# Optimization experiments

Measured on AMD Instinct MI355X. Metric: run time of the kernel, lower is better.

Reference implementation:

```python
import jax, jax.numpy as jnp
import numpy as np

B, S, D = 4, 2048, 1024
E, K, H = 8, 2, 4096


def setup_inputs() -> dict:
    key = jax.random.key(0)
    ks = jax.random.split(key, 8)
    sd = 1.0 / np.sqrt(D)
    sh = 1.0 / np.sqrt(H)
    x = jax.random.normal(ks[0], (B, S, D), dtype=jnp.float32)
    gate_w = jax.random.normal(ks[1], (D, E), dtype=jnp.float32) * sd
    gate_b = jnp.zeros((E,), dtype=jnp.float32)
    w1 = jax.random.normal(ks[2], (E, D, H), dtype=jnp.float32) * sd
    b1 = jnp.zeros((E, H), dtype=jnp.float32)
    w2 = jax.random.normal(ks[3], (E, H, D), dtype=jnp.float32) * sh
    b2 = jnp.zeros((E, D), dtype=jnp.float32)
    return {"x": x, "gate_w": gate_w, "gate_b": gate_b,
            "w1": w1, "b1": b1, "w2": w2, "b2": b2}


def reference(x, gate_w, gate_b, w1, b1, w2, b2):
    # gate logits [B,S,E]
    logits = jnp.einsum('bsd,de->bse', x, gate_w) + gate_b
    # top-k over experts, softmax over the k selected (dim=2), in float32
    weights, selected = jax.lax.top_k(logits, K)            # [B,S,K]
    weights = jax.nn.softmax(weights.astype(jnp.float32), axis=-1).astype(x.dtype)
    out = jnp.zeros_like(x)
    for i in range(E):
        # per-token combine weight for expert i (0 if not routed here)
        w_i = jnp.sum(jnp.where(selected == i, weights, 0.0), axis=-1)  # [B,S]
        h = jax.nn.gelu(jnp.einsum('bsd,dh->bsh', x, w1[i]) + b1[i])    # [B,S,H]
        y = jnp.einsum('bsh,hd->bsd', h, w2[i]) + b2[i]                  # [B,S,D]
        out = out + w_i[..., None] * y
    return out
```

## Files before the change

### kernel.cpp

```cpp
#include <hip/hip_runtime.h>
#include <hip/hip_bf16.h>
#include <stdint.h>

#define T_TOK 8192
#define D_DIM 1024
#define E_NUM 8
#define H_DIM 4096
#define WL_MAX 136

typedef short bf16x8 __attribute__((ext_vector_type(8)));
typedef float f32x4 __attribute__((ext_vector_type(4)));
typedef unsigned short usv8 __attribute__((ext_vector_type(8)));

#define AS1 __attribute__((address_space(1)))
#define AS3 __attribute__((address_space(3)))

__device__ __forceinline__ unsigned short f2b(float f) {
  union { float f; uint32_t u; } v; v.f = f;
  uint32_t r = (v.u + 0x7fffu + ((v.u >> 16) & 1u)) >> 16;
  return (unsigned short)r;
}

__device__ __forceinline__ float gelu_tanh(float x) {
  float u = 0.7978845608028654f * (x + 0.044715f * x * x * x);
  u = fminf(fmaxf(u, -15.f), 15.f);
  float e = __expf(2.f * u);
  float t = (e - 1.f) / (e + 1.f);
  return 0.5f * x * (1.f + t);
}

__device__ __forceinline__ void gload_lds16(const void* g, void* l) {
  __builtin_amdgcn_global_load_lds((const AS1 uint32_t*)g, (AS3 uint32_t*)l, 16, 0, 0);
}

__global__ __launch_bounds__(256) void moe_gate_conv(const float* __restrict__ x,
                                                     const float* __restrict__ gw,
                                                     const float* __restrict__ gb,
                                                     unsigned short* __restrict__ xb,
                                                     int2* __restrict__ sel,
                                                     float2* __restrict__ wts,
                                                     int* __restrict__ meta) {
  int lane = threadIdx.x & 63;
  int t = blockIdx.x * 4 + (threadIdx.x >> 6);
  const float* xr = x + (size_t)t * D_DIM;
  unsigned short* xo = xb + (size_t)t * D_DIM;
  float acc[8];
#pragma unroll
  for (int e = 0; e < 8; e++) acc[e] = 0.f;
#pragma unroll
  for (int i = 0; i < 4; i++) {
    int d0 = lane * 4 + i * 256;
    float4 xv = *(const float4*)(xr + d0);
    ushort4 o;
    o.x = f2b(xv.x); o.y = f2b(xv.y); o.z = f2b(xv.z); o.w = f2b(xv.w);
    *(ushort4*)(xo + d0) = o;
    const float* gp = gw + (size_t)d0 * 8;
    float xs[4] = {xv.x, xv.y, xv.z, xv.w};
#pragma unroll
    for (int j = 0; j < 4; j++) {
#pragma unroll
      for (int e = 0; e < 8; e++) acc[e] += xs[j] * gp[j * 8 + e];
    }
  }
#pragma unroll
  for (int off = 32; off > 0; off >>= 1) {
#pragma unroll
    for (int e = 0; e < 8; e++) acc[e] += __shfl_xor(acc[e], off);
  }
  if (lane == 0) {
    float lg[8];
#pragma unroll
    for (int e = 0; e < 8; e++) lg[e] = acc[e] + gb[e];
    int e0 = 0; float b0 = lg[0];
#pragma unroll
    for (int e = 1; e < 8; e++) if (lg[e] > b0) { b0 = lg[e]; e0 = e; }
    int e1 = -1; float b1v = -1e30f;
#pragma unroll
    for (int e = 0; e < 8; e++) if (e != e0 && lg[e] > b1v) { b1v = lg[e]; e1 = e; }
    float d = __expf(b1v - b0);
    float w0 = 1.f / (1.f + d), w1 = d / (1.f + d);
    sel[t] = make_int2(e0, e1);
    wts[t] = make_float2(w0, w1);
    atomicAdd(&meta[e0], 1);
    atomicAdd(&meta[e1], 1);
  }
}

__global__ __launch_bounds__(256) void moe_transpose(const float* __restrict__ in,
                                                     unsigned short* __restrict__ out,
                                                     int R, int C) {
  int e = blockIdx.z;
  int c0 = blockIdx.x * 64, r0 = blockIdx.y * 64;
  __shared__ float tile[64][65];
  const float* ine = in + (size_t)e * R * C;
  unsigned short* oute = out + (size_t)e * R * C;
  int tr = threadIdx.x >> 2;
  int tc4 = (threadIdx.x & 3) * 16;
#pragma unroll
  for (int p = 0; p < 4; p++) {
    int c = tc4 + p * 4;
    float4 v = *(const float4*)(ine + (size_t)(r0 + tr) * C + c0 + c);
    tile[tr][c] = v.x; tile[tr][c + 1] = v.y; tile[tr][c + 2] = v.z; tile[tr][c + 3] = v.w;
  }
  __syncthreads();
#pragma unroll
  for (int p = 0; p < 4; p++) {
    int rr = tc4 + p * 4;
    ushort4 o;
    o.x = f2b(tile[rr + 0][tr]);
    o.y = f2b(tile[rr + 1][tr]);
    o.z = f2b(tile[rr + 2][tr]);
    o.w = f2b(tile[rr + 3][tr]);
    *(ushort4*)(oute + (size_t)(c0 + tr) * R + r0 + rr) = o;
  }
}

__global__ void moe_scan(int* meta, int2* wl) {
  if (threadIdx.x == 0 && blockIdx.x == 0) {
    int o = 0;
    for (int e = 0; e < 8; e++) { meta[8 + e] = o; meta[20 + e] = o; o += meta[e]; }
    meta[16] = o;
    int w = 0;
    for (int e = 0; e < 8; e++)
      for (int m0 = 0; m0 < meta[e]; m0 += 128) wl[w++] = make_int2(e, m0);
    meta[17] = w;
  }
}

__global__ __launch_bounds__(256) void moe_scatter(const int2* __restrict__ sel,
                                                   int* __restrict__ meta,
                                                   int* __restrict__ token_id,
                                                   int2* __restrict__ pos) {
  int t = blockIdx.x * 256 + threadIdx.x;
  if (t >= T_TOK) return;
  int2 s = sel[t];
  int p0 = atomicAdd(&meta[20 + s.x], 1); token_id[p0] = t;
  int p1 = atomicAdd(&meta[20 + s.y], 1); token_id[p1] = t;
  pos[t] = make_int2(p0, p1);
}

__global__ __launch_bounds__(256) void moe_gemm1(const unsigned short* __restrict__ xb,
                                                 const unsigned short* __restrict__ w1t,
                                                 const float* __restrict__ b1,
                                                 const int* __restrict__ meta,
                                                 const int2* __restrict__ wl,
                                                 const int* __restrict__ token_id,
                                                 unsigned short* __restrict__ hbuf) {
  int wi = blockIdx.y;
  if (wi >= meta[17]) return;
  int e = wl[wi].x, m0 = wl[wi].y;
  int seg = meta[8 + e], ne = meta[9 + e] - seg;
  int n0 = blockIdx.x * 128;
  const unsigned short* wB = w1t + (size_t)e * H_DIM * D_DIM;

  __shared__ unsigned short As[2][4096];
  __shared__ unsigned short Bs[2][4096];

  int tid = threadIdx.x, lane = tid & 63, wv = tid >> 6;
  const unsigned short* aptr[2];
  const unsigned short* bptr[2];
#pragma unroll
  for (int q = 0; q < 2; q++) {
    int chunk = (wv + 4 * q) * 64 + lane;
    int row = chunk >> 2;
    int ko = (chunk & 3) * 8;
    int gi = m0 + row; if (gi >= ne) gi = m0;
    int tok = token_id[seg + gi];
    aptr[q] = xb + (size_t)tok * D_DIM + ko;
    bptr[q] = wB + (size_t)(n0 + row) * D_DIM + ko;
  }
  auto stage = [&](int buf, int kt) {
#pragma unroll
    for (int q = 0; q < 2; q++) {
      gload_lds16(aptr[q] + kt * 32, &As[buf][(wv + 4 * q) * 512]);
      gload_lds16(bptr[q] + kt * 32, &Bs[buf][(wv + 4 * q) * 512]);
    }
  };

  f32x4 acc[4][4] = {};
  int wr = wv >> 1, wc = wv & 1;
  int abase = (wr * 64 + (lane & 15)) * 32 + (lane >> 4) * 8;
  int bbase = (wc * 64 + (lane & 15)) * 32 + (lane >> 4) * 8;

  stage(0, 0);
  __syncthreads();
  const int nk = D_DIM / 32;
  for (int kt = 0; kt < nk; ++kt) {
    int cur = kt & 1;
    if (kt + 1 < nk) stage(cur ^ 1, kt + 1);
    bf16x8 af[4], bfr[4];
#pragma unroll
    for (int m = 0; m < 4; m++) af[m] = *(const bf16x8*)&As[cur][abase + m * 512];
#pragma unroll
    for (int n = 0; n < 4; n++) bfr[n] = *(const bf16x8*)&Bs[cur][bbase + n * 512];
#pragma unroll
    for (int m = 0; m < 4; m++)
#pragma unroll
      for (int n = 0; n < 4; n++)
        acc[m][n] = __builtin_amdgcn_mfma_f32_16x16x32_bf16(af[m], bfr[n], acc[m][n], 0, 0, 0);
    __syncthreads();
  }

  int rbase = wr * 64 + (lane >> 4) * 4;
  int cbase = n0 + wc * 64 + (lane & 15);
  const float* b1e = b1 + (size_t)e * H_DIM + cbase;
  float bv[4];
#pragma unroll
  for (int n = 0; n < 4; n++) bv[n] = b1e[n * 16];
#pragma unroll
  for (int m = 0; m < 4; m++) {
#pragma unroll
    for (int j = 0; j < 4; j++) {
      int gi = m0 + rbase + m * 16 + j;
      if (gi < ne) {
        unsigned short* hrow = hbuf + (size_t)(seg + gi) * H_DIM + cbase;
#pragma unroll
        for (int n = 0; n < 4; n++) {
          float v = acc[m][n][j] + bv[n];
          hrow[n * 16] = f2b(gelu_tanh(v));
        }
      }
    }
  }
}

__global__ __launch_bounds__(256) void moe_gemm2(const unsigned short* __restrict__ hbuf,
                                                 const unsigned short* __restrict__ w2t,
                                                 const float* __restrict__ b2,
                                                 const int* __restrict__ meta,
                                                 const int2* __restrict__ wl,
                                                 float* __restrict__ y) {
  int wi = blockIdx.y;
  if (wi >= meta[17]) return;
  int e = wl[wi].x, m0 = wl[wi].y;
  int seg = meta[8 + e], ne = meta[9 + e] - seg;
  int n0 = blockIdx.x * 128;
  const unsigned short* wB = w2t + (size_t)e * D_DIM * H_DIM;

  __shared__ unsigned short As[2][4096];
  __shared__ unsigned short Bs[2][4096];

  int tid = threadIdx.x, lane = tid & 63, wv = tid >> 6;
  const unsigned short* aptr[2];
  const unsigned short* bptr[2];
#pragma unroll
  for (int q = 0; q < 2; q++) {
    int chunk = (wv + 4 * q) * 64 + lane;
    int row = chunk >> 2;
    int ko = (chunk & 3) * 8;
    int gi = m0 + row; if (gi >= ne) gi = m0;
    aptr[q] = hbuf + (size_t)(seg + gi) * H_DIM + ko;
    bptr[q] = wB + (size_t)(n0 + row) * H_DIM + ko;
  }
  auto stage = [&](int buf, int kt) {
#pragma unroll
    for (int q = 0; q < 2; q++) {
      gload_lds16(aptr[q] + kt * 32, &As[buf][(wv + 4 * q) * 512]);
      gload_lds16(bptr[q] + kt * 32, &Bs[buf][(wv + 4 * q) * 512]);
    }
  };

  f32x4 acc[4][4] = {};
  int wr = wv >> 1, wc = wv & 1;
  int abase = (wr * 64 + (lane & 15)) * 32 + (lane >> 4) * 8;
  int bbase = (wc * 64 + (lane & 15)) * 32 + (lane >> 4) * 8;

  stage(0, 0);
  __syncthreads();
  const int nk = H_DIM / 32;
  for (int kt = 0; kt < nk; ++kt) {
    int cur = kt & 1;
    if (kt + 1 < nk) stage(cur ^ 1, kt + 1);
    bf16x8 af[4], bfr[4];
#pragma unroll
    for (int m = 0; m < 4; m++) af[m] = *(const bf16x8*)&As[cur][abase + m * 512];
#pragma unroll
    for (int n = 0; n < 4; n++) bfr[n] = *(const bf16x8*)&Bs[cur][bbase + n * 512];
#pragma unroll
    for (int m = 0; m < 4; m++)
#pragma unroll
      for (int n = 0; n < 4; n++)
        acc[m][n] = __builtin_amdgcn_mfma_f32_16x16x32_bf16(af[m], bfr[n], acc[m][n], 0, 0, 0);
    __syncthreads();
  }

  int rbase = wr * 64 + (lane >> 4) * 4;
  int cbase = n0 + wc * 64 + (lane & 15);
  const float* b2e = b2 + (size_t)e * D_DIM + cbase;
  float bv[4];
#pragma unroll
  for (int n = 0; n < 4; n++) bv[n] = b2e[n * 16];
#pragma unroll
  for (int m = 0; m < 4; m++) {
#pragma unroll
    for (int j = 0; j < 4; j++) {
      int gi = m0 + rbase + m * 16 + j;
      if (gi < ne) {
        float* yrow = y + (size_t)(seg + gi) * D_DIM + cbase;
#pragma unroll
        for (int n = 0; n < 4; n++)
          yrow[n * 16] = acc[m][n][j] + bv[n];
      }
    }
  }
}

__global__ __launch_bounds__(256) void moe_combine(const float* __restrict__ y,
                                                   const int2* __restrict__ pos,
                                                   const float2* __restrict__ wts,
                                                   float* __restrict__ out) {
  int i = blockIdx.x * 256 + threadIdx.x;
  int idx = i * 4;
  int t = idx >> 10, d = idx & 1023;
  int2 p = pos[t];
  float2 w = wts[t];
  float4 a = *(const float4*)(y + (size_t)p.x * D_DIM + d);
  float4 b = *(const float4*)(y + (size_t)p.y * D_DIM + d);
  float4 o;
  o.x = w.x * a.x + w.y * b.x;
  o.y = w.x * a.y + w.y * b.y;
  o.z = w.x * a.z + w.y * b.z;
  o.w = w.x * a.w + w.y * b.w;
  *(float4*)(out + idx) = o;
}

extern "C" void kernel_launch(void* const* d_in, const int* in_sizes, int n_in,
                              void* d_out, int out_size, void* d_ws, size_t ws_size,
                              hipStream_t stream) {
  const float* x      = (const float*)d_in[0];
  const float* gate_w = (const float*)d_in[1];
  const float* gate_b = (const float*)d_in[2];
  const float* w1     = (const float*)d_in[3];
  const float* b1     = (const float*)d_in[4];
  const float* w2     = (const float*)d_in[5];
  const float* b2     = (const float*)d_in[6];
  float* out = (float*)d_out;

  uint8_t* ws = (uint8_t*)d_ws;
  unsigned short* hbuf = (unsigned short*)(ws);
  unsigned short* xb   = (unsigned short*)(ws + 134217728ull);
  unsigned short* w1t  = (unsigned short*)(ws + 150994944ull);
  float*          yb   = (float*)         (ws + 150994944ull);
  unsigned short* w2t  = (unsigned short*)(ws + 218103808ull);
  int*    token_id = (int*)  (ws + 285212672ull);
  int2*   pos      = (int2*) (ws + 285278208ull);
  float2* wts      = (float2*)(ws + 285343744ull);
  int2*   sel      = (int2*) (ws + 285409280ull);
  int*    meta     = (int*)  (ws + 285474816ull);
  int2*   wl       = (int2*) (ws + 285475328ull);

  hipMemsetAsync(meta, 0, 512, stream);

  moe_gate_conv<<<dim3(T_TOK / 4), 256, 0, stream>>>(x, gate_w, gate_b, xb, sel, wts, meta);
  moe_transpose<<<dim3(H_DIM / 64, D_DIM / 64, E_NUM), 256, 0, stream>>>(w1, w1t, D_DIM, H_DIM);
  moe_transpose<<<dim3(D_DIM / 64, H_DIM / 64, E_NUM), 256, 0, stream>>>(w2, w2t, H_DIM, D_DIM);
  moe_scan<<<1, 64, 0, stream>>>(meta, wl);
  moe_scatter<<<dim3(T_TOK / 256), 256, 0, stream>>>(sel, meta, token_id, pos);
  moe_gemm1<<<dim3(H_DIM / 128, WL_MAX), 256, 0, stream>>>(xb, w1t, b1, meta, wl, token_id, hbuf);
  moe_gemm2<<<dim3(D_DIM / 128, WL_MAX), 256, 0, stream>>>(hbuf, w2t, b2, meta, wl, yb);
  moe_combine<<<dim3((T_TOK * D_DIM) / 1024), 256, 0, stream>>>(yb, pos, wts, out);
}
```

Baseline: 879.0 us.

## Merge expert GEMMs into one templated 256x256 kernel with triple-buffered pipeline and split-K

Replaces the two 128x128 double-buffered expert GEMMs with one templated kernel that uses 256x256 tiles, 512 threads and a three-stage LDS pipeline with explicit waitcnt and barriers. The work list now advances in 256-row chunks. The second GEMM splits K in two and accumulates into a zeroed y buffer with atomic adds. The larger tiles and deeper prefetch are meant to raise data reuse and hide load latency. In exchange the code adds a memset, atomic traffic on the output, more padding waste in partial M tiles, and higher register and LDS pressure.

After: 934.5 us. 6.3% more time.

```diff
diff --git a/kernel.cpp b/kernel.cpp
--- a/kernel.cpp
+++ b/kernel.cpp
@@ -6,11 +6,10 @@
 #define D_DIM 1024
 #define E_NUM 8
 #define H_DIM 4096
-#define WL_MAX 136
+#define WL_MAX 72
 
 typedef short bf16x8 __attribute__((ext_vector_type(8)));
 typedef float f32x4 __attribute__((ext_vector_type(4)));
-typedef unsigned short usv8 __attribute__((ext_vector_type(8)));
 
 #define AS1 __attribute__((address_space(1)))
 #define AS3 __attribute__((address_space(3)))
@@ -122,7 +121,7 @@
     meta[16] = o;
     int w = 0;
     for (int e = 0; e < 8; e++)
-      for (int m0 = 0; m0 < meta[e]; m0 += 128) wl[w++] = make_int2(e, m0);
+      for (int m0 = 0; m0 < meta[e]; m0 += 256) wl[w++] = make_int2(e, m0);
     meta[17] = w;
   }
 }
@@ -139,167 +138,111 @@
   pos[t] = make_int2(p0, p1);
 }
 
-__global__ __launch_bounds__(256) void moe_gemm1(const unsigned short* __restrict__ xb,
-                                                 const unsigned short* __restrict__ w1t,
-                                                 const float* __restrict__ b1,
-                                                 const int* __restrict__ meta,
-                                                 const int2* __restrict__ wl,
-                                                 const int* __restrict__ token_id,
-                                                 unsigned short* __restrict__ hbuf) {
+template<int MODE>
+__global__ __launch_bounds__(512, 2) void moe_gemm_pipe(
+    const unsigned short* __restrict__ Amat,
+    const unsigned short* __restrict__ Bmat,
+    const float* __restrict__ bias,
+    const int* __restrict__ meta,
+    const int2* __restrict__ wl,
+    const int* __restrict__ token_id,
+    unsigned short* __restrict__ hout,
+    float* __restrict__ yout) {
+  constexpr int KLEN = MODE ? 4096 : 1024;
+  constexpr int NK   = MODE ? 64 : 32;
+  constexpr int NOUT = MODE ? 1024 : 4096;
+
   int wi = blockIdx.y;
   if (wi >= meta[17]) return;
   int e = wl[wi].x, m0 = wl[wi].y;
   int seg = meta[8 + e], ne = meta[9 + e] - seg;
-  int n0 = blockIdx.x * 128;
-  const unsigned short* wB = w1t + (size_t)e * H_DIM * D_DIM;
-
-  __shared__ unsigned short As[2][4096];
-  __shared__ unsigned short Bs[2][4096];
-
-  int tid = threadIdx.x, lane = tid & 63, wv = tid >> 6;
-  const unsigned short* aptr[2];
-  const unsigned short* bptr[2];
-#pragma unroll
-  for (int q = 0; q < 2; q++) {
-    int chunk = (wv + 4 * q) * 64 + lane;
+  int n0, ks;
+  if (MODE) { n0 = (int)(blockIdx.x >> 1) * 256; ks = blockIdx.x & 1; }
+  else      { n0 = blockIdx.x * 256; ks = 0; }
+  const int kbase = ks * 2048;
+
+  __shared__ unsigned short As[3][8192];
+  __shared__ unsigned short Bs[3][8192];
+
+  int tid = threadIdx.x, lane = tid & 63, w = tid >> 6;
+  int wm = w >> 2, wn = w & 3;
+
+  const unsigned short* aSrc[2];
+  const unsigned short* bSrc[2];
+#pragma unroll
+  for (int q = 0; q < 2; ++q) {
+    int chunk = (w * 2 + q) * 64 + lane;
     int row = chunk >> 2;
     int ko = (chunk & 3) * 8;
     int gi = m0 + row; if (gi >= ne) gi = m0;
-    int tok = token_id[seg + gi];
-    aptr[q] = xb + (size_t)tok * D_DIM + ko;
-    bptr[q] = wB + (size_t)(n0 + row) * D_DIM + ko;
-  }
-  auto stage = [&](int buf, int kt) {
-#pragma unroll
-    for (int q = 0; q < 2; q++) {
-      gload_lds16(aptr[q] + kt * 32, &As[buf][(wv + 4 * q) * 512]);
-      gload_lds16(bptr[q] + kt * 32, &Bs[buf][(wv + 4 * q) * 512]);
+    if (MODE) aSrc[q] = Amat + (size_t)(seg + gi) * KLEN + kbase + ko;
+    else      aSrc[q] = Amat + (size_t)token_id[seg + gi] * KLEN + ko;
+    bSrc[q] = Bmat + (size_t)e * (4096 * 1024) + (size_t)(n0 + row) * KLEN + kbase + ko;
+  }
+
+  auto STAGE = [&](int buf, int kt) {
+#pragma unroll
+    for (int q = 0; q < 2; ++q) {
+      gload_lds16(aSrc[q] + kt * 32, &As[buf][(w * 2 + q) * 512]);
+      gload_lds16(bSrc[q] + kt * 32, &Bs[buf][(w * 2 + q) * 512]);
     }
   };
 
-  f32x4 acc[4][4] = {};
-  int wr = wv >> 1, wc = wv & 1;
-  int abase = (wr * 64 + (lane & 15)) * 32 + (lane >> 4) * 8;
-  int bbase = (wc * 64 + (lane & 15)) * 32 + (lane >> 4) * 8;
-
-  stage(0, 0);
-  __syncthreads();
-  const int nk = D_DIM / 32;
-  for (int kt = 0; kt < nk; ++kt) {
-    int cur = kt & 1;
-    if (kt + 1 < nk) stage(cur ^ 1, kt + 1);
-    bf16x8 af[4], bfr[4];
-#pragma unroll
-    for (int m = 0; m < 4; m++) af[m] = *(const bf16x8*)&As[cur][abase + m * 512];
-#pragma unroll
-    for (int n = 0; n < 4; n++) bfr[n] = *(const bf16x8*)&Bs[cur][bbase + n * 512];
-#pragma unroll
-    for (int m = 0; m < 4; m++)
-#pragma unroll
-      for (int n = 0; n < 4; n++)
-        acc[m][n] = __builtin_amdgcn_mfma_f32_16x16x32_bf16(af[m], bfr[n], acc[m][n], 0, 0, 0);
-    __syncthreads();
-  }
-
-  int rbase = wr * 64 + (lane >> 4) * 4;
-  int cbase = n0 + wc * 64 + (lane & 15);
-  const float* b1e = b1 + (size_t)e * H_DIM + cbase;
-  float bv[4];
-#pragma unroll
-  for (int n = 0; n < 4; n++) bv[n] = b1e[n * 16];
-#pragma unroll
-  for (int m = 0; m < 4; m++) {
-#pragma unroll
-    for (int j = 0; j < 4; j++) {
-      int gi = m0 + rbase + m * 16 + j;
+  f32x4 acc[8][4] = {};
+  const int aoff = (wm * 128 + (lane & 15)) * 32 + (lane >> 4) * 8;
+  const int boff = (wn * 64 + (lane & 15)) * 32 + (lane >> 4) * 8;
+
+  STAGE(0, 0); STAGE(1, 1); STAGE(2, 2);
+
+  int t = 0, cur = 0;
+#define GSTEP(WAITSTR, DOSTAGE) do { \
+    asm volatile("s_waitcnt " WAITSTR ::: "memory"); \
+    __builtin_amdgcn_s_barrier(); \
+    __builtin_amdgcn_sched_barrier(0); \
+    bf16x8 af[8], bv8[4]; \
+    _Pragma("unroll") for (int mf = 0; mf < 8; ++mf) af[mf] = *(const bf16x8*)&As[cur][aoff + mf * 512]; \
+    _Pragma("unroll") for (int nf = 0; nf < 4; ++nf) bv8[nf] = *(const bf16x8*)&Bs[cur][boff + nf * 512]; \
+    asm volatile("s_waitcnt lgkmcnt(0)" ::: "memory"); \
+    __builtin_amdgcn_sched_barrier(0); \
+    __builtin_amdgcn_s_barrier(); \
+    __builtin_amdgcn_sched_barrier(0); \
+    if (DOSTAGE) STAGE(cur, t + 3); \
+    _Pragma("unroll") for (int mf = 0; mf < 8; ++mf) \
+      _Pragma("unroll") for (int nf = 0; nf < 4; ++nf) \
+        acc[mf][nf] = __builtin_amdgcn_mfma_f32_16x16x32_bf16(af[mf], bv8[nf], acc[mf][nf], 0, 0, 0); \
+    cur = (cur == 2) ? 0 : cur + 1; \
+    ++t; \
+  } while (0)
+
+  for (int it = 0; it < NK - 3; ++it) GSTEP("vmcnt(8)", true);
+  GSTEP("vmcnt(8)", false);
+  GSTEP("vmcnt(4)", false);
+  GSTEP("vmcnt(0)", false);
+#undef GSTEP
+
+  int rb = wm * 128 + (lane >> 4) * 4;
+  int cb = n0 + wn * 64 + (lane & 15);
+  const float* be = bias + (size_t)e * NOUT + cb;
+  float bvv[4];
+#pragma unroll
+  for (int nf = 0; nf < 4; ++nf) bvv[nf] = (MODE && ks) ? 0.f : be[nf * 16];
+#pragma unroll
+  for (int mf = 0; mf < 8; ++mf) {
+#pragma unroll
+    for (int j = 0; j < 4; ++j) {
+      int gi = m0 + rb + mf * 16 + j;
       if (gi < ne) {
-        unsigned short* hrow = hbuf + (size_t)(seg + gi) * H_DIM + cbase;
-#pragma unroll
-        for (int n = 0; n < 4; n++) {
-          float v = acc[m][n][j] + bv[n];
-          hrow[n * 16] = f2b(gelu_tanh(v));
+        if (MODE) {
+          float* yrow = yout + (size_t)(seg + gi) * 1024 + cb;
+#pragma unroll
+          for (int nf = 0; nf < 4; ++nf)
+            atomicAdd(&yrow[nf * 16], acc[mf][nf][j] + bvv[nf]);
+        } else {
+          unsigned short* hrow = hout + (size_t)(seg + gi) * 4096 + cb;
+#pragma unroll
+          for (int nf = 0; nf < 4; ++nf)
+            hrow[nf * 16] = f2b(gelu_tanh(acc[mf][nf][j] + bvv[nf]));
         }
-      }
-    }
-  }
-}
-
-__global__ __launch_bounds__(256) void moe_gemm2(const unsigned short* __restrict__ hbuf,
-                                                 const unsigned short* __restrict__ w2t,
-                                                 const float* __restrict__ b2,
-                                                 const int* __restrict__ meta,
-                                                 const int2* __restrict__ wl,
-                                                 float* __restrict__ y) {
-  int wi = blockIdx.y;
-  if (wi >= meta[17]) return;
-  int e = wl[wi].x, m0 = wl[wi].y;
-  int seg = meta[8 + e], ne = meta[9 + e] - seg;
-  int n0 = blockIdx.x * 128;
-  const unsigned short* wB = w2t + (size_t)e * D_DIM * H_DIM;
-
-  __shared__ unsigned short As[2][4096];
-  __shared__ unsigned short Bs[2][4096];
-
-  int tid = threadIdx.x, lane = tid & 63, wv = tid >> 6;
-  const unsigned short* aptr[2];
-  const unsigned short* bptr[2];
-#pragma unroll
-  for (int q = 0; q < 2; q++) {
-    int chunk = (wv + 4 * q) * 64 + lane;
-    int row = chunk >> 2;
-    int ko = (chunk & 3) * 8;
-    int gi = m0 + row; if (gi >= ne) gi = m0;
-    aptr[q] = hbuf + (size_t)(seg + gi) * H_DIM + ko;
-    bptr[q] = wB + (size_t)(n0 + row) * H_DIM + ko;
-  }
-  auto stage = [&](int buf, int kt) {
-#pragma unroll
-    for (int q = 0; q < 2; q++) {
-      gload_lds16(aptr[q] + kt * 32, &As[buf][(wv + 4 * q) * 512]);
-      gload_lds16(bptr[q] + kt * 32, &Bs[buf][(wv + 4 * q) * 512]);
-    }
-  };
-
-  f32x4 acc[4][4] = {};
-  int wr = wv >> 1, wc = wv & 1;
-  int abase = (wr * 64 + (lane & 15)) * 32 + (lane >> 4) * 8;
-  int bbase = (wc * 64 + (lane & 15)) * 32 + (lane >> 4) * 8;
-
-  stage(0, 0);
-  __syncthreads();
-  const int nk = H_DIM / 32;
-  for (int kt = 0; kt < nk; ++kt) {
-    int cur = kt & 1;
-    if (kt + 1 < nk) stage(cur ^ 1, kt + 1);
-    bf16x8 af[4], bfr[4];
-#pragma unroll
-    for (int m = 0; m < 4; m++) af[m] = *(const bf16x8*)&As[cur][abase + m * 512];
-#pragma unroll
-    for (int n = 0; n < 4; n++) bfr[n] = *(const bf16x8*)&Bs[cur][bbase + n * 512];
-#pragma unroll
-    for (int m = 0; m < 4; m++)
-#pragma unroll
-      for (int n = 0; n < 4; n++)
-        acc[m][n] = __builtin_amdgcn_mfma_f32_16x16x32_bf16(af[m], bfr[n], acc[m][n], 0, 0, 0);
-    __syncthreads();
-  }
-
-  int rbase = wr * 64 + (lane >> 4) * 4;
-  int cbase = n0 + wc * 64 + (lane & 15);
-  const float* b2e = b2 + (size_t)e * D_DIM + cbase;
-  float bv[4];
-#pragma unroll
-  for (int n = 0; n < 4; n++) bv[n] = b2e[n * 16];
-#pragma unroll
-  for (int m = 0; m < 4; m++) {
-#pragma unroll
-    for (int j = 0; j < 4; j++) {
-      int gi = m0 + rbase + m * 16 + j;
-      if (gi < ne) {
-        float* yrow = y + (size_t)(seg + gi) * D_DIM + cbase;
-#pragma unroll
-        for (int n = 0; n < 4; n++)
-          yrow[n * 16] = acc[m][n][j] + bv[n];
       }
     }
   }
@@ -356,7 +299,14 @@
   moe_transpose<<<dim3(D_DIM / 64, H_DIM / 64, E_NUM), 256, 0, stream>>>(w2, w2t, H_DIM, D_DIM);
   moe_scan<<<1, 64, 0, stream>>>(meta, wl);
   moe_scatter<<<dim3(T_TOK / 256), 256, 0, stream>>>(sel, meta, token_id, pos);
-  moe_gemm1<<<dim3(H_DIM / 128, WL_MAX), 256, 0, stream>>>(xb, w1t, b1, meta, wl, token_id, hbuf);
-  moe_gemm2<<<dim3(D_DIM / 128, WL_MAX), 256, 0, stream>>>(hbuf, w2t, b2, meta, wl, yb);
+
+  moe_gemm_pipe<0><<<dim3(H_DIM / 256, WL_MAX), 512, 0, stream>>>(
+      xb, w1t, b1, meta, wl, token_id, hbuf, nullptr);
+
+  hipMemsetAsync(yb, 0, (size_t)T_TOK * 2 * D_DIM * sizeof(float), stream);
+
+  moe_gemm_pipe<1><<<dim3((D_DIM / 256) * 2, WL_MAX), 512, 0, stream>>>(
+      hbuf, w2t, b2, meta, wl, token_id, nullptr, yb);
+
   moe_combine<<<dim3((T_TOK * D_DIM) / 1024), 256, 0, stream>>>(yb, pos, wts, out);
 }
```

## Fuse weighted combine into GEMM2 via atomics and remap grid for XCD locality

Applied to the files above, without the earlier changes.

Removes the separate combine kernel and the fp32 y buffer. A new init kernel writes the weighted bias into out, and gemm2 then atomically adds weight*acc straight into out rows indexed by token. Both GEMMs also switch to a flattened 1D grid whose low three bits pick a chiplet group, so work-list tiles are spread across XCDs with N tiles grouped together for cache reuse. This saves the y write and read traffic, at the cost of many scalar fp32 atomics and summation order that is no longer deterministic.

New measurement: 889.3 us. Within noise of the previous version (+1.2%).

```diff
diff --git a/kernel.cpp b/kernel.cpp
--- a/kernel.cpp
+++ b/kernel.cpp
@@ -6,11 +6,11 @@
 #define D_DIM 1024
 #define E_NUM 8
 #define H_DIM 4096
-#define WL_MAX 136
+#define NPAD 144
+#define PPX (NPAD / 8)
 
 typedef short bf16x8 __attribute__((ext_vector_type(8)));
 typedef float f32x4 __attribute__((ext_vector_type(4)));
-typedef unsigned short usv8 __attribute__((ext_vector_type(8)));
 
 #define AS1 __attribute__((address_space(1)))
 #define AS3 __attribute__((address_space(3)))
@@ -128,15 +128,34 @@
 }
 
 __global__ __launch_bounds__(256) void moe_scatter(const int2* __restrict__ sel,
+                                                   const float2* __restrict__ wts,
                                                    int* __restrict__ meta,
                                                    int* __restrict__ token_id,
-                                                   int2* __restrict__ pos) {
+                                                   float* __restrict__ weightv) {
   int t = blockIdx.x * 256 + threadIdx.x;
   if (t >= T_TOK) return;
   int2 s = sel[t];
-  int p0 = atomicAdd(&meta[20 + s.x], 1); token_id[p0] = t;
-  int p1 = atomicAdd(&meta[20 + s.y], 1); token_id[p1] = t;
-  pos[t] = make_int2(p0, p1);
+  float2 w = wts[t];
+  int p0 = atomicAdd(&meta[20 + s.x], 1); token_id[p0] = t; weightv[p0] = w.x;
+  int p1 = atomicAdd(&meta[20 + s.y], 1); token_id[p1] = t; weightv[p1] = w.y;
+}
+
+__global__ __launch_bounds__(256) void moe_outinit(const int2* __restrict__ sel,
+                                                   const float2* __restrict__ wts,
+                                                   const float* __restrict__ b2,
+                                                   float* __restrict__ out) {
+  int t = blockIdx.x;
+  int d = threadIdx.x * 4;
+  int2 s = sel[t];
+  float2 w = wts[t];
+  float4 a = *(const float4*)(b2 + (size_t)s.x * D_DIM + d);
+  float4 b = *(const float4*)(b2 + (size_t)s.y * D_DIM + d);
+  float4 o;
+  o.x = w.x * a.x + w.y * b.x;
+  o.y = w.x * a.y + w.y * b.y;
+  o.z = w.x * a.z + w.y * b.z;
+  o.w = w.x * a.w + w.y * b.w;
+  *(float4*)(out + (size_t)t * D_DIM + d) = o;
 }
 
 __global__ __launch_bounds__(256) void moe_gemm1(const unsigned short* __restrict__ xb,
@@ -146,11 +165,14 @@
                                                  const int2* __restrict__ wl,
                                                  const int* __restrict__ token_id,
                                                  unsigned short* __restrict__ hbuf) {
-  int wi = blockIdx.y;
+  int b = blockIdx.x;
+  int c = b & 7, u = b >> 3;
+  int n = u & 31, ps = u >> 5;
+  int wi = c * PPX + ps;
   if (wi >= meta[17]) return;
   int e = wl[wi].x, m0 = wl[wi].y;
   int seg = meta[8 + e], ne = meta[9 + e] - seg;
-  int n0 = blockIdx.x * 128;
+  int n0 = n * 128;
   const unsigned short* wB = w1t + (size_t)e * H_DIM * D_DIM;
 
   __shared__ unsigned short As[2][4096];
@@ -192,12 +214,12 @@
 #pragma unroll
     for (int m = 0; m < 4; m++) af[m] = *(const bf16x8*)&As[cur][abase + m * 512];
 #pragma unroll
-    for (int n = 0; n < 4; n++) bfr[n] = *(const bf16x8*)&Bs[cur][bbase + n * 512];
+    for (int nn = 0; nn < 4; nn++) bfr[nn] = *(const bf16x8*)&Bs[cur][bbase + nn * 512];
 #pragma unroll
     for (int m = 0; m < 4; m++)
 #pragma unroll
-      for (int n = 0; n < 4; n++)
-        acc[m][n] = __builtin_amdgcn_mfma_f32_16x16x32_bf16(af[m], bfr[n], acc[m][n], 0, 0, 0);
+      for (int nn = 0; nn < 4; nn++)
+        acc[m][nn] = __builtin_amdgcn_mfma_f32_16x16x32_bf16(af[m], bfr[nn], acc[m][nn], 0, 0, 0);
     __syncthreads();
   }
 
@@ -206,7 +228,7 @@
   const float* b1e = b1 + (size_t)e * H_DIM + cbase;
   float bv[4];
 #pragma unroll
-  for (int n = 0; n < 4; n++) bv[n] = b1e[n * 16];
+  for (int nn = 0; nn < 4; nn++) bv[nn] = b1e[nn * 16];
 #pragma unroll
   for (int m = 0; m < 4; m++) {
 #pragma unroll
@@ -215,9 +237,9 @@
       if (gi < ne) {
         unsigned short* hrow = hbuf + (size_t)(seg + gi) * H_DIM + cbase;
 #pragma unroll
-        for (int n = 0; n < 4; n++) {
-          float v = acc[m][n][j] + bv[n];
-          hrow[n * 16] = f2b(gelu_tanh(v));
+        for (int nn = 0; nn < 4; nn++) {
+          float v = acc[m][nn][j] + bv[nn];
+          hrow[nn * 16] = f2b(gelu_tanh(v));
         }
       }
     }
@@ -226,15 +248,19 @@
 
 __global__ __launch_bounds__(256) void moe_gemm2(const unsigned short* __restrict__ hbuf,
                                                  const unsigned short* __restrict__ w2t,
-                                                 const float* __restrict__ b2,
                                                  const int* __restrict__ meta,
                                                  const int2* __restrict__ wl,
-                                                 float* __restrict__ y) {
-  int wi = blockIdx.y;
+                                                 const int* __restrict__ token_id,
+                                                 const float* __restrict__ weightv,
+                                                 float* __restrict__ out) {
+  int b = blockIdx.x;
+  int c = b & 7, u = b >> 3;
+  int n = u & 7, ps = u >> 3;
+  int wi = c * PPX + ps;
   if (wi >= meta[17]) return;
   int e = wl[wi].x, m0 = wl[wi].y;
   int seg = meta[8 + e], ne = meta[9 + e] - seg;
-  int n0 = blockIdx.x * 128;
+  int n0 = n * 128;
   const unsigned short* wB = w2t + (size_t)e * D_DIM * H_DIM;
 
   __shared__ unsigned short As[2][4096];
@@ -275,53 +301,33 @@
 #pragma unroll
     for (int m = 0; m < 4; m++) af[m] = *(const bf16x8*)&As[cur][abase + m * 512];
 #pragma unroll
-    for (int n = 0; n < 4; n++) bfr[n] = *(const bf16x8*)&Bs[cur][bbase + n * 512];
+    for (int nn = 0; nn < 4; nn++) bfr[nn] = *(const bf16x8*)&Bs[cur][bbase + nn * 512];
 #pragma unroll
     for (int m = 0; m < 4; m++)
 #pragma unroll
-      for (int n = 0; n < 4; n++)
-        acc[m][n] = __builtin_amdgcn_mfma_f32_16x16x32_bf16(af[m], bfr[n], acc[m][n], 0, 0, 0);
+      for (int nn = 0; nn < 4; nn++)
+        acc[m][nn] = __builtin_amdgcn_mfma_f32_16x16x32_bf16(af[m], bfr[nn], acc[m][nn], 0, 0, 0);
     __syncthreads();
   }
 
   int rbase = wr * 64 + (lane >> 4) * 4;
   int cbase = n0 + wc * 64 + (lane & 15);
-  const float* b2e = b2 + (size_t)e * D_DIM + cbase;
-  float bv[4];
-#pragma unroll
-  for (int n = 0; n < 4; n++) bv[n] = b2e[n * 16];
 #pragma unroll
   for (int m = 0; m < 4; m++) {
 #pragma unroll
     for (int j = 0; j < 4; j++) {
       int gi = m0 + rbase + m * 16 + j;
       if (gi < ne) {
-        float* yrow = y + (size_t)(seg + gi) * D_DIM + cbase;
-#pragma unroll
-        for (int n = 0; n < 4; n++)
-          yrow[n * 16] = acc[m][n][j] + bv[n];
+        int p = seg + gi;
+        int tok = token_id[p];
+        float wt = weightv[p];
+        float* orow = out + (size_t)tok * D_DIM + cbase;
+#pragma unroll
+        for (int nn = 0; nn < 4; nn++)
+          atomicAdd(&orow[nn * 16], wt * acc[m][nn][j]);
       }
     }
   }
-}
-
-__global__ __launch_bounds__(256) void moe_combine(const float* __restrict__ y,
-                                                   const int2* __restrict__ pos,
-                                                   const float2* __restrict__ wts,
-                                                   float* __restrict__ out) {
-  int i = blockIdx.x * 256 + threadIdx.x;
-  int idx = i * 4;
-  int t = idx >> 10, d = idx & 1023;
-  int2 p = pos[t];
-  float2 w = wts[t];
-  float4 a = *(const float4*)(y + (size_t)p.x * D_DIM + d);
-  float4 b = *(const float4*)(y + (size_t)p.y * D_DIM + d);
-  float4 o;
-  o.x = w.x * a.x + w.y * b.x;
-  o.y = w.x * a.y + w.y * b.y;
-  o.z = w.x * a.z + w.y * b.z;
-  o.w = w.x * a.w + w.y * b.w;
-  *(float4*)(out + idx) = o;
 }
 
 extern "C" void kernel_launch(void* const* d_in, const int* in_sizes, int n_in,
@@ -340,10 +346,9 @@
   unsigned short* hbuf = (unsigned short*)(ws);
   unsigned short* xb   = (unsigned short*)(ws + 134217728ull);
   unsigned short* w1t  = (unsigned short*)(ws + 150994944ull);
-  float*          yb   = (float*)         (ws + 150994944ull);
   unsigned short* w2t  = (unsigned short*)(ws + 218103808ull);
   int*    token_id = (int*)  (ws + 285212672ull);
-  int2*   pos      = (int2*) (ws + 285278208ull);
+  float*  weightv  = (float*)(ws + 285278208ull);
   float2* wts      = (float2*)(ws + 285343744ull);
   int2*   sel      = (int2*) (ws + 285409280ull);
   int*    meta     = (int*)  (ws + 285474816ull);
@@ -355,8 +360,9 @@
   moe_transpose<<<dim3(H_DIM / 64, D_DIM / 64, E_NUM), 256, 0, stream>>>(w1, w1t, D_DIM, H_DIM);
   moe_transpose<<<dim3(D_DIM / 64, H_DIM / 64, E_NUM), 256, 0, stream>>>(w2, w2t, H_DIM, D_DIM);
   moe_scan<<<1, 64, 0, stream>>>(meta, wl);
-  moe_scatter<<<dim3(T_TOK / 256), 256, 0, stream>>>(sel, meta, token_id, pos);
-  moe_gemm1<<<dim3(H_DIM / 128, WL_MAX), 256, 0, stream>>>(xb, w1t, b1, meta, wl, token_id, hbuf);
-  moe_gemm2<<<dim3(D_DIM / 128, WL_MAX), 256, 0, stream>>>(hbuf, w2t, b2, meta, wl, yb);
-  moe_combine<<<dim3((T_TOK * D_DIM) / 1024), 256, 0, stream>>>(yb, pos, wts, out);
-}
+  moe_scatter<<<dim3(T_TOK / 256), 256, 0, stream>>>(sel, wts, meta, token_id, weightv);
+  moe_outinit<<<dim3(T_TOK), 256, 0, stream>>>(sel, wts, b2, out);
+
+  moe_gemm1<<<dim3(NPAD * 32), 256, 0, stream>>>(xb, w1t, b1, meta, wl, token_id, hbuf);
+  moe_gemm2<<<dim3(NPAD * 8), 256, 0, stream>>>(hbuf, w2t, meta, wl, token_id, weightv, out);
+}
```
